# Kernel optimization log

Measured on AMD Instinct MI355X. Metric: run time of the kernel, lower is better.

Reference implementation:

```python
import jax, jax.numpy as jnp
import numpy as np


def setup_inputs() -> dict:
    key = jax.random.key(0)
    k1, k2 = jax.random.split(key)
    # (t, h, w) per image/video; h, w divisible by spatial_merge_size=2
    grid_thw = jnp.asarray(np.array([[1, 64, 64], [4, 48, 48], [8, 32, 64], [16, 32, 32]], dtype=np.int64))
    num_grid_per_side = 35
    hidden = 1152
    pos_embed_weight = jax.random.normal(k1, (num_grid_per_side * num_grid_per_side, hidden), dtype=jnp.float32)
    quarter_head_dim = 32  # mrope_section [24,20,20] sums to 64 = 2*quarter_head_dim
    inv_freq = 1.0 / (10000.0 ** (jnp.arange(quarter_head_dim, dtype=jnp.float32) / quarter_head_dim))
    return {
        'grid_thw': grid_thw,
        'pos_embed_weight': pos_embed_weight,
        'inv_freq': inv_freq,
        'spatial_merge_size': 2,
        'num_grid_per_side': num_grid_per_side,
    }


def _forward(grid_np, pos_embed_weight, inv_freq, m, G):
    # grid_np: host numpy int array [num_images, 3] -> static per-image shapes
    D = pos_embed_weight.shape[-1]
    pieces = []
    coords_list = []
    for t, h, w in grid_np.tolist():
        # ---- 4-corner bilinear interpolation of pos embeddings ----
        h_idxs = jnp.linspace(0.0, G - 1, h)
        w_idxs = jnp.linspace(0.0, G - 1, w)
        hf = h_idxs.astype(jnp.int32)
        wf = w_idxs.astype(jnp.int32)
        hc = jnp.minimum(hf + 1, G - 1)
        wc = jnp.minimum(wf + 1, G - 1)
        dh = h_idxs - hf.astype(h_idxs.dtype)
        dw = w_idxs - wf.astype(w_idxs.dtype)
        idx = jnp.stack([
            (hf[:, None] * G + wf[None, :]).reshape(-1),
            (hf[:, None] * G + wc[None, :]).reshape(-1),
            (hc[:, None] * G + wf[None, :]).reshape(-1),
            (hc[:, None] * G + wc[None, :]).reshape(-1),
        ], 0)  # [4, h*w]
        wts = jnp.stack([
            ((1 - dh)[:, None] * (1 - dw)[None, :]).reshape(-1),
            ((1 - dh)[:, None] * dw[None, :]).reshape(-1),
            (dh[:, None] * (1 - dw)[None, :]).reshape(-1),
            (dh[:, None] * dw[None, :]).reshape(-1),
        ], 0).astype(pos_embed_weight.dtype)  # [4, h*w]
        pe = (pos_embed_weight[idx] * wts[:, :, None]).sum(0)  # [h*w, D]
        # ---- spatial-merge reshuffle, repeated over t frames ----
        pe = jnp.tile(pe, (t, 1)).reshape(t, h // m, m, w // m, m, D)
        pe = pe.transpose(0, 1, 3, 2, 4, 5).reshape(-1, D)
        pieces.append(pe)
        # ---- (row, col) position ids in merged-block order ----
        br = jnp.arange(h // m)
        bc = jnp.arange(w // m)
        im = jnp.arange(m)
        row = br[:, None, None, None] * m + im[None, None, :, None]
        col = bc[None, :, None, None] * m + im[None, None, None, :]
        row = jnp.broadcast_to(row, (h // m, w // m, m, m)).reshape(-1)
        col = jnp.broadcast_to(col, (h // m, w // m, m, m)).reshape(-1)
        coords = jnp.stack([row, col], -1)  # [h*w, 2]
        coords = jnp.tile(coords, (t, 1))   # [t*h*w, 2]
        coords_list.append(coords)
    patch_pos_embeds = jnp.concatenate(pieces, 0)   # [total_tokens, D]
    pos_ids = jnp.concatenate(coords_list, 0)       # [total_tokens, 2]
    max_hw = int(grid_np[:, 1:].max())
    seq = jnp.arange(max_hw, dtype=jnp.float32)
    freqs = seq[:, None] * inv_freq[None, :]        # [max_hw, Q]
    embeddings = freqs[pos_ids].reshape(pos_ids.shape[0], -1)  # [T, 2Q]
    # MRoPE section interleave: freqs_3d[0..2] are identical copies of
    # `embeddings`, so replacing strided slices of freqs_t with slices of the
    # other copies is a mathematical no-op: freqs_t == embeddings.
    emb = jnp.concatenate([embeddings, embeddings], -1)  # [T, head_dim]
    return patch_pos_embeds, jnp.cos(emb), jnp.sin(emb)


def reference(grid_thw, pos_embed_weight, inv_freq, spatial_merge_size, num_grid_per_side):
    grid_np = np.asarray(grid_thw)  # int grid sizes are static metadata
    return _forward(grid_np, pos_embed_weight, inv_freq, int(spatial_merge_size), int(num_grid_per_side))
```

## Files before the change

kernel.cpp:

```cpp
#include <hip/hip_runtime.h>


typedef float fx4 __attribute__((ext_vector_type(4)));

__device__ __forceinline__ void nt_store4(float* p, fx4 v) {
    __builtin_nontemporal_store(v, (fx4*)p);
}

template <int T, int H, int W, int OFF>
__device__ __forceinline__ void patch_body(int b, const float* __restrict__ tab,
                                           float* __restrict__ out) {
    constexpr int C4 = 1152 / 4;
    constexpr int HW = H * W;
    constexpr int WB = W / 2;

    int idx = b * 256 + (int)threadIdx.x;
    int tok = idx / C4;
    int c4  = idx - tok * C4;

    int j  = tok & 1;
    int i  = (tok >> 1) & 1;
    int blk = tok >> 2;
    int bw = blk % WB;
    int bh = blk / WB;
    int row = (bh << 1) + i;
    int col = (bw << 1) + j;

    float hx = (float)row * (float)(34.0 / (H - 1));
    float wx = (float)col * (float)(34.0 / (W - 1));
    int hf = (int)hx, wf = (int)wx;
    float dh = hx - (float)hf, dw = wx - (float)wf;
    int hc = min(hf + 1, 34), wc = min(wf + 1, 34);

    float w00 = (1.f - dh) * (1.f - dw);
    float w01 = (1.f - dh) * dw;
    float w10 = dh * (1.f - dw);
    float w11 = dh * dw;

    const fx4 a = *((const fx4*)(tab + (hf * 35 + wf) * 1152) + c4);
    const fx4 bq= *((const fx4*)(tab + (hf * 35 + wc) * 1152) + c4);
    const fx4 c = *((const fx4*)(tab + (hc * 35 + wf) * 1152) + c4);
    const fx4 d = *((const fx4*)(tab + (hc * 35 + wc) * 1152) + c4);

    fx4 o = w00 * a + w01 * bq + w10 * c + w11 * d;

    float* dst = out + (size_t)(OFF + tok) * 1152 + (c4 << 2);
    #pragma unroll
    for (int f = 0; f < T; ++f)
        nt_store4(dst + (size_t)f * (HW * 1152), o);
}

template <int T, int H, int W, int OFF>
__device__ __forceinline__ void rope_body(int b, const float* __restrict__ invf,
                                          float* __restrict__ cosO,
                                          float* __restrict__ sinO) {
    constexpr int HW = H * W;
    constexpr int WB = W / 2;

    int idx = b * 256 + (int)threadIdx.x;
    int tok = idx >> 4;
    int l4  = idx & 15;
    int rem = tok % HW;

    int j  = rem & 1;
    int i  = (rem >> 1) & 1;
    int blk = rem >> 2;
    int bw = blk % WB;
    int bh = blk / WB;
    int row = (bh << 1) + i;
    int col = (bw << 1) + j;

    float fp = (float)((l4 < 8) ? row : col);
    fx4 iv = ((const fx4*)invf)[l4 & 7];

    float s0, c0, s1, c1, s2, c2, s3, c3;
    __sincosf(fp * iv.x, &s0, &c0);
    __sincosf(fp * iv.y, &s1, &c1);
    __sincosf(fp * iv.z, &s2, &c2);
    __sincosf(fp * iv.w, &s3, &c3);
    fx4 cv = {c0, c1, c2, c3};
    fx4 sv = {s0, s1, s2, s3};

    size_t base = (size_t)(OFF + tok) * 128 + (l4 << 2);
    nt_store4(cosO + base,      cv);
    nt_store4(cosO + base + 64, cv);
    nt_store4(sinO + base,      sv);
    nt_store4(sinO + base + 64, sv);
}

__global__ __launch_bounds__(256) void fused_kernel(
    const float* __restrict__ tab, const float* __restrict__ invf,
    float* __restrict__ out, float* __restrict__ cosO, float* __restrict__ sinO)
{
    int b = (int)blockIdx.x;
    if      (b < 1152)  patch_body<16,32, 32, 29696>(b,         tab, out);
    else if (b < 3456)  patch_body<8, 32, 64, 13312>(b - 1152,  tab, out);
    else if (b < 6048)  patch_body<4, 48, 48, 4096> (b - 3456,  tab, out);
    else if (b < 7072)  rope_body<16,32, 32, 29696> (b - 6048,  invf, cosO, sinO);
    else if (b < 8096)  rope_body<8, 32, 64, 13312> (b - 7072,  invf, cosO, sinO);
    else if (b < 8672)  rope_body<4, 48, 48, 4096>  (b - 8096,  invf, cosO, sinO);
    else if (b < 8928)  rope_body<1, 64, 64, 0>     (b - 8672,  invf, cosO, sinO);
    else                patch_body<1, 64, 64, 0>    (b - 8928,  tab, out);
}

extern "C" void kernel_launch(void* const* d_in, const int* in_sizes, int n_in,
                              void* d_out, int out_size, void* d_ws, size_t ws_size,
                              hipStream_t stream) {
    const float* tab  = (const float*)d_in[1];
    const float* invf = (const float*)d_in[2];
    float* out = (float*)d_out;

    constexpr size_t NTOK = 46080;
    float* cosO = out + NTOK * 1152;
    float* sinO = cosO + NTOK * 128;

    fused_kernel<<<13536, 256, 0, stream>>>(tab, invf, out, cosO, sinO);
}
```

Measured before the change: 55.96 us.

## Split patch embedding work into channel chunks for table cache locality

The patch-embedding work is reorganised so the 1152-wide hidden dimension is cut into 8 chunks of 36 float4 columns. All tokens of all images are processed for one chunk before the next chunk starts. The intent is to keep each chunk's slice of the 35x35 position table small enough to stay resident in cache, which cuts repeated table reads. Each row of 36 float4s is a 576-byte segment, so the stores become less contiguous than full 4.6KB rows, and the rope blocks are moved to the end of the grid.

```diff
diff --git a/kernel.cpp b/kernel.cpp
--- a/kernel.cpp
+++ b/kernel.cpp
@@ -8,15 +8,16 @@
 }
 
 template <int T, int H, int W, int OFF>
-__device__ __forceinline__ void patch_body(int b, const float* __restrict__ tab,
+__device__ __forceinline__ void patch_body(int r, int chunk,
+                                           const float* __restrict__ tab,
                                            float* __restrict__ out) {
-    constexpr int C4 = 1152 / 4;
     constexpr int HW = H * W;
     constexpr int WB = W / 2;
 
-    int idx = b * 256 + (int)threadIdx.x;
-    int tok = idx / C4;
-    int c4  = idx - tok * C4;
+    int idx = r * 256 + (int)threadIdx.x;
+    int tok = idx / 36;
+    int c4w = idx - tok * 36;
+    int c4  = chunk * 36 + c4w;
 
     int j  = tok & 1;
     int i  = (tok >> 1) & 1;
@@ -93,14 +94,20 @@
     float* __restrict__ out, float* __restrict__ cosO, float* __restrict__ sinO)
 {
     int b = (int)blockIdx.x;
-    if      (b < 1152)  patch_body<16,32, 32, 29696>(b,         tab, out);
-    else if (b < 3456)  patch_body<8, 32, 64, 13312>(b - 1152,  tab, out);
-    else if (b < 6048)  patch_body<4, 48, 48, 4096> (b - 3456,  tab, out);
-    else if (b < 7072)  rope_body<16,32, 32, 29696> (b - 6048,  invf, cosO, sinO);
-    else if (b < 8096)  rope_body<8, 32, 64, 13312> (b - 7072,  invf, cosO, sinO);
-    else if (b < 8672)  rope_body<4, 48, 48, 4096>  (b - 8096,  invf, cosO, sinO);
-    else if (b < 8928)  rope_body<1, 64, 64, 0>     (b - 8672,  invf, cosO, sinO);
-    else                patch_body<1, 64, 64, 0>    (b - 8928,  tab, out);
+    if (b < 10656) {
+        int chunk = b / 1332;
+        int r     = b - chunk * 1332;
+        if      (r < 144) patch_body<16,32, 32, 29696>(r,       chunk, tab, out);
+        else if (r < 432) patch_body<8, 32, 64, 13312>(r - 144, chunk, tab, out);
+        else if (r < 756) patch_body<4, 48, 48, 4096> (r - 432, chunk, tab, out);
+        else              patch_body<1, 64, 64, 0>    (r - 756, chunk, tab, out);
+    } else {
+        int r = b - 10656;
+        if      (r < 1024) rope_body<16,32, 32, 29696>(r,        invf, cosO, sinO);
+        else if (r < 2048) rope_body<8, 32, 64, 13312>(r - 1024, invf, cosO, sinO);
+        else if (r < 2624) rope_body<4, 48, 48, 4096> (r - 2048, invf, cosO, sinO);
+        else               rope_body<1, 64, 64, 0>    (r - 2624, invf, cosO, sinO);
+    }
 }
 
 extern "C" void kernel_launch(void* const* d_in, const int* in_sizes, int n_in,
```

After: 58.52 us. +4.6%, slower.

## Use grid-stride spans per segment and rebalance block counts across work types

Applied to the files above, without the earlier changes.

Replaces the one-element-per-thread mapping with per-block spans that each block walks in a strided loop. The grid shrinks and block counts are re-proportioned across the pe and rope segments, with the cost-heavier T=16/T=8 pieces given more blocks. The rope path now has each thread cover one 4-float chunk of the full 128-wide row (two stores instead of four), which doubles the rope thread count and removes duplicate sincos reuse. The aim is to cut block scheduling overhead and tail imbalance. The risk is lower parallelism per segment and loop overhead.

```diff
diff --git a/kernel.cpp b/kernel.cpp
--- a/kernel.cpp
+++ b/kernel.cpp
@@ -7,85 +7,91 @@
     __builtin_nontemporal_store(v, (fx4*)p);
 }
 
-template <int T, int H, int W, int OFF>
-__device__ __forceinline__ void patch_body(int b, const float* __restrict__ tab,
-                                           float* __restrict__ out) {
-    constexpr int C4 = 1152 / 4;
-    constexpr int HW = H * W;
-    constexpr int WB = W / 2;
+template <int T, int H, int W, int OFF, int NBLK>
+__device__ __forceinline__ void pe_body(int r, const float* __restrict__ tab,
+                                        float* __restrict__ out) {
+    constexpr int HW    = H * W;
+    constexpr int TASKS = HW * 288;
+    constexpr int SPAN  = (TASKS + NBLK - 1) / NBLK;
+    constexpr int WB    = W / 2;
 
-    int idx = b * 256 + (int)threadIdx.x;
-    int tok = idx / C4;
-    int c4  = idx - tok * C4;
+    int t1 = min(r * SPAN + SPAN, TASKS);
+    for (int t = r * SPAN + (int)threadIdx.x; t < t1; t += 256) {
+        int tok = t / 288;
+        int c4  = t - tok * 288;
 
-    int j  = tok & 1;
-    int i  = (tok >> 1) & 1;
-    int blk = tok >> 2;
-    int bw = blk % WB;
-    int bh = blk / WB;
-    int row = (bh << 1) + i;
-    int col = (bw << 1) + j;
+        int j  = tok & 1;
+        int i  = (tok >> 1) & 1;
+        int blk = tok >> 2;
+        int bw = blk % WB;
+        int bh = blk / WB;
+        int row = (bh << 1) + i;
+        int col = (bw << 1) + j;
 
-    float hx = (float)row * (float)(34.0 / (H - 1));
-    float wx = (float)col * (float)(34.0 / (W - 1));
-    int hf = (int)hx, wf = (int)wx;
-    float dh = hx - (float)hf, dw = wx - (float)wf;
-    int hc = min(hf + 1, 34), wc = min(wf + 1, 34);
+        float hx = (float)row * (float)(34.0 / (H - 1));
+        float wx = (float)col * (float)(34.0 / (W - 1));
+        int hf = (int)hx, wf = (int)wx;
+        float dh = hx - (float)hf, dw = wx - (float)wf;
+        int hc = min(hf + 1, 34), wc = min(wf + 1, 34);
 
-    float w00 = (1.f - dh) * (1.f - dw);
-    float w01 = (1.f - dh) * dw;
-    float w10 = dh * (1.f - dw);
-    float w11 = dh * dw;
+        float w00 = (1.f - dh) * (1.f - dw);
+        float w01 = (1.f - dh) * dw;
+        float w10 = dh * (1.f - dw);
+        float w11 = dh * dw;
 
-    const fx4 a = *((const fx4*)(tab + (hf * 35 + wf) * 1152) + c4);
-    const fx4 bq= *((const fx4*)(tab + (hf * 35 + wc) * 1152) + c4);
-    const fx4 c = *((const fx4*)(tab + (hc * 35 + wf) * 1152) + c4);
-    const fx4 d = *((const fx4*)(tab + (hc * 35 + wc) * 1152) + c4);
+        const fx4 a = *((const fx4*)(tab + (hf * 35 + wf) * 1152) + c4);
+        const fx4 bq= *((const fx4*)(tab + (hf * 35 + wc) * 1152) + c4);
+        const fx4 c = *((const fx4*)(tab + (hc * 35 + wf) * 1152) + c4);
+        const fx4 d = *((const fx4*)(tab + (hc * 35 + wc) * 1152) + c4);
 
-    fx4 o = w00 * a + w01 * bq + w10 * c + w11 * d;
+        fx4 o = w00 * a + w01 * bq + w10 * c + w11 * d;
 
-    float* dst = out + (size_t)(OFF + tok) * 1152 + (c4 << 2);
-    #pragma unroll
-    for (int f = 0; f < T; ++f)
-        nt_store4(dst + (size_t)f * (HW * 1152), o);
+        float* dst = out + (size_t)(OFF + tok) * 1152 + (c4 << 2);
+        #pragma unroll
+        for (int f = 0; f < T; ++f)
+            nt_store4(dst + (size_t)f * (HW * 1152), o);
+    }
 }
 
-template <int T, int H, int W, int OFF>
-__device__ __forceinline__ void rope_body(int b, const float* __restrict__ invf,
+template <int T, int H, int W, int OFF, int NBLK>
+__device__ __forceinline__ void rope_body(int r, const float* __restrict__ invf,
                                           float* __restrict__ cosO,
                                           float* __restrict__ sinO) {
-    constexpr int HW = H * W;
-    constexpr int WB = W / 2;
+    constexpr int HW   = H * W;
+    constexpr int CH   = T * HW * 32;
+    constexpr int SPAN = CH / NBLK;
+    constexpr int WB   = W / 2;
 
-    int idx = b * 256 + (int)threadIdx.x;
-    int tok = idx >> 4;
-    int l4  = idx & 15;
-    int rem = tok % HW;
+    int q1 = r * SPAN + SPAN;
+    for (int q = r * SPAN + (int)threadIdx.x; q < q1; q += 256) {
+        int tokl = q >> 5;
+        int l4   = q & 31;
+        int lq   = l4 & 15;
+        int rem  = tokl % HW;
 
-    int j  = rem & 1;
-    int i  = (rem >> 1) & 1;
-    int blk = rem >> 2;
-    int bw = blk % WB;
-    int bh = blk / WB;
-    int row = (bh << 1) + i;
-    int col = (bw << 1) + j;
+        int j  = rem & 1;
+        int i  = (rem >> 1) & 1;
+        int blk = rem >> 2;
+        int bw = blk % WB;
+        int bh = blk / WB;
+        int row = (bh << 1) + i;
+        int col = (bw << 1) + j;
 
-    float fp = (float)((l4 < 8) ? row : col);
-    fx4 iv = ((const fx4*)invf)[l4 & 7];
+        float fp = (float)((lq < 8) ? row : col);
+        fx4 iv = ((const fx4*)invf)[lq & 7];
 
-    float s0, c0, s1, c1, s2, c2, s3, c3;
-    __sincosf(fp * iv.x, &s0, &c0);
-    __sincosf(fp * iv.y, &s1, &c1);
-    __sincosf(fp * iv.z, &s2, &c2);
-    __sincosf(fp * iv.w, &s3, &c3);
-    fx4 cv = {c0, c1, c2, c3};
-    fx4 sv = {s0, s1, s2, s3};
+        float s0, c0, s1, c1, s2, c2, s3, c3;
+        __sincosf(fp * iv.x, &s0, &c0);
+        __sincosf(fp * iv.y, &s1, &c1);
+        __sincosf(fp * iv.z, &s2, &c2);
+        __sincosf(fp * iv.w, &s3, &c3);
+        fx4 cv = {c0, c1, c2, c3};
+        fx4 sv = {s0, s1, s2, s3};
 
-    size_t base = (size_t)(OFF + tok) * 128 + (l4 << 2);
-    nt_store4(cosO + base,      cv);
-    nt_store4(cosO + base + 64, cv);
-    nt_store4(sinO + base,      sv);
-    nt_store4(sinO + base + 64, sv);
+        size_t base = (size_t)(OFF + tokl) * 128 + (l4 << 2);
+        nt_store4(cosO + base, cv);
+        nt_store4(sinO + base, sv);
+    }
 }
 
 __global__ __launch_bounds__(256) void fused_kernel(
@@ -93,14 +99,14 @@
     float* __restrict__ out, float* __restrict__ cosO, float* __restrict__ sinO)
 {
     int b = (int)blockIdx.x;
-    if      (b < 1152)  patch_body<16,32, 32, 29696>(b,         tab, out);
-    else if (b < 3456)  patch_body<8, 32, 64, 13312>(b - 1152,  tab, out);
-    else if (b < 6048)  patch_body<4, 48, 48, 4096> (b - 3456,  tab, out);
-    else if (b < 7072)  rope_body<16,32, 32, 29696> (b - 6048,  invf, cosO, sinO);
-    else if (b < 8096)  rope_body<8, 32, 64, 13312> (b - 7072,  invf, cosO, sinO);
-    else if (b < 8672)  rope_body<4, 48, 48, 4096>  (b - 8096,  invf, cosO, sinO);
-    else if (b < 8928)  rope_body<1, 64, 64, 0>     (b - 8672,  invf, cosO, sinO);
-    else                patch_body<1, 64, 64, 0>    (b - 8928,  tab, out);
+    if      (b < 320)  pe_body<1, 64, 64, 0,     320> (b,        tab, out);
+    else if (b < 1024) pe_body<4, 48, 48, 4096,  704> (b - 320,  tab, out);
+    else if (b < 2240) pe_body<8, 32, 64, 13312, 1216>(b - 1024, tab, out);
+    else if (b < 3456) pe_body<16,32, 32, 29696, 1216>(b - 2240, tab, out);
+    else if (b < 3520) rope_body<1, 64, 64, 0,     64> (b - 3456, invf, cosO, sinO);
+    else if (b < 3664) rope_body<4, 48, 48, 4096,  144>(b - 3520, invf, cosO, sinO);
+    else if (b < 3920) rope_body<8, 32, 64, 13312, 256>(b - 3664, invf, cosO, sinO);
+    else               rope_body<16,32, 32, 29696, 256>(b - 3920, invf, cosO, sinO);
 }
 
 extern "C" void kernel_launch(void* const* d_in, const int* in_sizes, int n_in,
@@ -114,5 +120,5 @@
     float* cosO = out + NTOK * 1152;
     float* sinO = cosO + NTOK * 128;
 
-    fused_kernel<<<13536, 256, 0, stream>>>(tab, invf, out, cosO, sinO);
+    fused_kernel<<<4176, 256, 0, stream>>>(tab, invf, out, cosO, sinO);
 }
```

Measured after the change: 72.41 us. 1.29x slower.

## Stage interpolation table rows in LDS per output row and channel slice

Applied to the files above, without the earlier changes.

Each patch block now handles one output image row and a 72-channel slice. It first copies the two needed table rows (floor and ceil of the height position) for all 35 grid columns into shared memory, then computes every output column of that row from LDS. This replaces four global gathers per output element with one cooperative staged load per block, cutting redundant table reads and shrinking the grid. The cost is a barrier per block, staging loads of columns the row may not use, and fewer, larger blocks. Output stays write-bandwidth bound.

```diff
diff --git a/kernel.cpp b/kernel.cpp
--- a/kernel.cpp
+++ b/kernel.cpp
@@ -10,44 +10,61 @@
 template <int T, int H, int W, int OFF>
 __device__ __forceinline__ void patch_body(int b, const float* __restrict__ tab,
                                            float* __restrict__ out) {
-    constexpr int C4 = 1152 / 4;
     constexpr int HW = H * W;
     constexpr int WB = W / 2;
 
-    int idx = b * 256 + (int)threadIdx.x;
-    int tok = idx / C4;
-    int c4  = idx - tok * C4;
+    __shared__ float lds[2 * 35 * 72];
 
-    int j  = tok & 1;
-    int i  = (tok >> 1) & 1;
-    int blk = tok >> 2;
-    int bw = blk % WB;
-    int bh = blk / WB;
-    int row = (bh << 1) + i;
-    int col = (bw << 1) + j;
+    int hrow  = b >> 4;
+    int c0    = (b & 15) * 72;
 
-    float hx = (float)row * (float)(34.0 / (H - 1));
-    float wx = (float)col * (float)(34.0 / (W - 1));
-    int hf = (int)hx, wf = (int)wx;
-    float dh = hx - (float)hf, dw = wx - (float)wf;
-    int hc = min(hf + 1, 34), wc = min(wf + 1, 34);
+    float hx = (float)hrow * (float)(34.0 / (H - 1));
+    int   hf = (int)hx;
+    float dh = hx - (float)hf;
+    int   hc = min(hf + 1, 34);
 
-    float w00 = (1.f - dh) * (1.f - dw);
-    float w01 = (1.f - dh) * dw;
-    float w10 = dh * (1.f - dw);
-    float w11 = dh * dw;
+    for (int s = (int)threadIdx.x; s < 2 * 35 * 18; s += 256) {
+        int half = s / (35 * 18);
+        int r2   = s - half * (35 * 18);
+        int wcol = r2 / 18;
+        int q    = r2 - wcol * 18;
+        int hrt  = half ? hc : hf;
+        fx4 v = *((const fx4*)(tab + (size_t)(hrt * 35 + wcol) * 1152 + c0) + q);
+        *((fx4*)&lds[half * (35 * 72) + wcol * 72 + (q << 2)]) = v;
+    }
+    __syncthreads();
 
-    const fx4 a = *((const fx4*)(tab + (hf * 35 + wf) * 1152) + c4);
-    const fx4 bq= *((const fx4*)(tab + (hf * 35 + wc) * 1152) + c4);
-    const fx4 c = *((const fx4*)(tab + (hc * 35 + wf) * 1152) + c4);
-    const fx4 d = *((const fx4*)(tab + (hc * 35 + wc) * 1152) + c4);
+    float omdh = 1.f - dh;
 
-    fx4 o = w00 * a + w01 * bq + w10 * c + w11 * d;
+    for (int t = (int)threadIdx.x; t < W * 18; t += 256) {
+        int colw = t / 18;
+        int q    = t - colw * 18;
 
-    float* dst = out + (size_t)(OFF + tok) * 1152 + (c4 << 2);
-    #pragma unroll
-    for (int f = 0; f < T; ++f)
-        nt_store4(dst + (size_t)f * (HW * 1152), o);
+        float wx = (float)colw * (float)(34.0 / (W - 1));
+        int   wf = (int)wx;
+        float dw = wx - (float)wf;
+        int   wc = min(wf + 1, 34);
+
+        float w00 = omdh * (1.f - dw);
+        float w01 = omdh * dw;
+        float w10 = dh * (1.f - dw);
+        float w11 = dh * dw;
+
+        const fx4 a = *((const fx4*)&lds[            wf * 72 + (q << 2)]);
+        const fx4 bq= *((const fx4*)&lds[            wc * 72 + (q << 2)]);
+        const fx4 c = *((const fx4*)&lds[35 * 72 +   wf * 72 + (q << 2)]);
+        const fx4 d = *((const fx4*)&lds[35 * 72 +   wc * 72 + (q << 2)]);
+
+        fx4 o = w00 * a + w01 * bq + w10 * c + w11 * d;
+
+        int tok = (((hrow >> 1) * WB + (colw >> 1)) << 2)
+                + ((hrow & 1) << 1) + (colw & 1);
+
+        float* dst = out + (size_t)(OFF + tok) * 1152 + c0 + (q << 2);
+        #pragma unroll
+        for (int f = 0; f < T; ++f)
+            nt_store4(dst + (size_t)f * (HW * 1152), o);
+    }
 }
 
 template <int T, int H, int W, int OFF>
@@ -93,14 +110,14 @@
     float* __restrict__ out, float* __restrict__ cosO, float* __restrict__ sinO)
 {
     int b = (int)blockIdx.x;
-    if      (b < 1152)  patch_body<16,32, 32, 29696>(b,         tab, out);
-    else if (b < 3456)  patch_body<8, 32, 64, 13312>(b - 1152,  tab, out);
-    else if (b < 6048)  patch_body<4, 48, 48, 4096> (b - 3456,  tab, out);
-    else if (b < 7072)  rope_body<16,32, 32, 29696> (b - 6048,  invf, cosO, sinO);
-    else if (b < 8096)  rope_body<8, 32, 64, 13312> (b - 7072,  invf, cosO, sinO);
-    else if (b < 8672)  rope_body<4, 48, 48, 4096>  (b - 8096,  invf, cosO, sinO);
-    else if (b < 8928)  rope_body<1, 64, 64, 0>     (b - 8672,  invf, cosO, sinO);
-    else                patch_body<1, 64, 64, 0>    (b - 8928,  tab, out);
+    if      (b < 512)  patch_body<16,32, 32, 29696>(b,         tab, out);
+    else if (b < 1024) patch_body<8, 32, 64, 13312>(b - 512,   tab, out);
+    else if (b < 1792) patch_body<4, 48, 48, 4096> (b - 1024,  tab, out);
+    else if (b < 2816) rope_body<16,32, 32, 29696> (b - 1792,  invf, cosO, sinO);
+    else if (b < 3840) rope_body<8, 32, 64, 13312> (b - 2816,  invf, cosO, sinO);
+    else if (b < 4416) rope_body<4, 48, 48, 4096>  (b - 3840,  invf, cosO, sinO);
+    else if (b < 4672) rope_body<1, 64, 64, 0>     (b - 4416,  invf, cosO, sinO);
+    else               patch_body<1, 64, 64, 0>    (b - 4672,  tab, out);
 }
 
 extern "C" void kernel_launch(void* const* d_in, const int* in_sizes, int n_in,
@@ -114,5 +131,5 @@
     float* cosO = out + NTOK * 1152;
     float* sinO = cosO + NTOK * 128;
 
-    fused_kernel<<<13536, 256, 0, stream>>>(tab, invf, out, cosO, sinO);
+    fused_kernel<<<5696, 256, 0, stream>>>(tab, invf, out, cosO, sinO);
 }
```

After: 99.04 us. 1.77x slower.
